# Kernel tuning notes

Hardware: AMD Instinct MI355X
Metric: run time of the kernel (lower is better)

Reference implementation:

```python
import jax, jax.numpy as jnp
import numpy as np

N_EMBED = 384

def setup_inputs() -> dict:
    key = jax.random.key(0)
    kx, kq, kk, kv = jax.random.split(key, 4)
    B, T, C = 512, 256, N_EMBED
    H = 64
    scale = 1.0 / np.sqrt(C)  # param init scale, keep activations sane
    x = jax.random.normal(kx, (B, T, C), dtype=jnp.float32)
    Wq = jax.random.normal(kq, (C, H), dtype=jnp.float32) * scale
    Wk = jax.random.normal(kk, (C, H), dtype=jnp.float32) * scale
    Wv = jax.random.normal(kv, (C, H), dtype=jnp.float32) * scale
    return {"x": x, "Wq": Wq, "Wk": Wk, "Wv": Wv}

def reference(x, Wq, Wk, Wv):
    B, T, C = x.shape
    q = jnp.einsum('btc,ch->bth', x, Wq)
    k = jnp.einsum('btc,ch->bth', x, Wk)
    v = jnp.einsum('btc,ch->bth', x, Wv)
    # NOTE: original scales by C**-0.5 with C = n_embed (384), not head_size.
    wei = jnp.einsum('bth,bsh->bts', q, k) * (C ** -0.5)  # [B,T,T]
    causal = jnp.tril(jnp.ones((T, T), dtype=bool))
    wei = jnp.where(causal, wei, -jnp.inf)
    wei = jax.nn.softmax(wei, axis=-1)
    out = jnp.einsum('bts,bsh->bth', wei, v)  # [B,T,H]
    return out
```

## Files before the change

### kernel.cpp

```cpp
#include <hip/hip_runtime.h>
#include <hip/hip_bf16.h>


constexpr int BSZ  = 512;
constexpr int TT   = 256;
constexpr int CDIM = 384;
constexpr int HDIM = 64;
constexpr int NQKV = 192;
constexpr float SCALE = 0.051031036307982884f;
constexpr int BTST = 392;

typedef __attribute__((ext_vector_type(8))) short bf16x8;
typedef __attribute__((ext_vector_type(4))) float f32x4;

__device__ inline unsigned short f2bf(float f) {
    __hip_bfloat16 h = __float2bfloat16(f);
    return *(unsigned short*)&h;
}
__device__ inline bf16x8 pack8(float4 a, float4 b) {
    unsigned short p[8] = { f2bf(a.x), f2bf(a.y), f2bf(a.z), f2bf(a.w),
                            f2bf(b.x), f2bf(b.y), f2bf(b.z), f2bf(b.w) };
    return *(bf16x8*)p;
}

__global__ __launch_bounds__(256) void prep_bt(
    const float* __restrict__ Wq, const float* __restrict__ Wk,
    const float* __restrict__ Wv, unsigned short* __restrict__ bt)
{
    int idx = blockIdx.x * 256 + threadIdx.x;
    if (idx >= NQKV * CDIM) return;
    int n = idx / CDIM, k = idx - n * CDIM;
    const float* W = (n < 64) ? Wq : (n < 128) ? Wk : Wv;
    bt[idx] = f2bf(W[(size_t)k * HDIM + (n & 63)]);
}

__global__ __launch_bounds__(1024) void fused(
    const float* __restrict__ x, const unsigned short* __restrict__ bt,
    float* __restrict__ out)
{
    __shared__ __align__(16) unsigned short smem[NQKV * BTST];
    unsigned short* btl = smem;
    unsigned short* qs  = smem;
    unsigned short* kl  = smem + 16384;
    unsigned short* vt  = smem + 32768;

    const int b = blockIdx.x, tid = threadIdx.x;
    const int w = tid >> 6, lane = tid & 63;
    const int lr = lane & 15, lk = lane >> 4;
    const float* xb = x + (size_t)b * TT * CDIM;

    for (int i = tid; i < NQKV * CDIM / 8; i += 1024) {
        int row = i / 48, c8 = i - row * 48;
        *(uint4*)&btl[row * BTST + c8 * 8] = ((const uint4*)bt)[i];
    }
    __syncthreads();

    const float* xrow = xb + (size_t)(16 * w + lr) * CDIM + lk * 8;

    f32x4 acc[12];
    #pragma unroll
    for (int ni = 0; ni < 12; ++ni) acc[ni] = (f32x4){0.f, 0.f, 0.f, 0.f};

    float4 f0 = *(const float4*)&xrow[0];
    float4 f1 = *(const float4*)&xrow[4];
    #pragma unroll 2
    for (int ks = 0; ks < 12; ++ks) {
        float4 c0 = f0, c1 = f1;
        if (ks < 11) {
            f0 = *(const float4*)&xrow[(ks + 1) * 32];
            f1 = *(const float4*)&xrow[(ks + 1) * 32 + 4];
        }
        bf16x8 a = pack8(c0, c1);
        #pragma unroll
        for (int ni = 0; ni < 12; ++ni) {
            bf16x8 bb = *(const bf16x8*)&btl[(ni * 16 + lr) * BTST + ks * 32 + lk * 8];
            acc[ni] = __builtin_amdgcn_mfma_f32_16x16x32_bf16(a, bb, acc[ni], 0, 0, 0);
        }
    }
    __syncthreads();

    unsigned short* pq = qs + w * 1024;
    #pragma unroll
    for (int ni = 0; ni < 4; ++ni)
        #pragma unroll
        for (int r = 0; r < 4; ++r) {
            int qr = lk * 4 + r;
            int h  = ni * 16 + lr;
            pq[qr * 64 + (h ^ ((qr & 7) << 3))] = f2bf(acc[ni][r] * SCALE);
        }
    #pragma unroll
    for (int ni = 4; ni < 8; ++ni)
        #pragma unroll
        for (int r = 0; r < 4; ++r) {
            int row = 16 * w + lk * 4 + r;
            int c2  = (ni - 4) * 16 + lr;
            kl[row * 64 + (c2 ^ ((row & 7) << 3))] = f2bf(acc[ni][r]);
        }
    #pragma unroll
    for (int ni = 8; ni < 12; ++ni) {
        int h  = (ni - 8) * 16 + lr;
        int t0 = 16 * w + lk * 4;
        unsigned short pk[4];
        #pragma unroll
        for (int r = 0; r < 4; ++r) pk[r] = f2bf(acc[ni][r]);
        *(uint2*)&vt[h * 256 + (t0 ^ ((h & 7) << 3))] = *(uint2*)pk;
    }
    __syncthreads();

    const int q0 = 16 * w;
    bf16x8 qa[2];
    #pragma unroll
    for (int kc = 0; kc < 2; ++kc)
        qa[kc] = *(const bf16x8*)&pq[lr * 64 + ((kc * 32 + lk * 8) ^ ((lr & 7) << 3))];

    f32x4 oacc[4];
    float mrow[4], lpart[4];
    #pragma unroll
    for (int nh = 0; nh < 4; ++nh) oacc[nh] = (f32x4){0.f, 0.f, 0.f, 0.f};
    #pragma unroll
    for (int r = 0; r < 4; ++r) { mrow[r] = -INFINITY; lpart[r] = 0.f; }

    const int lastt = w >> 2;
    for (int st = 0; st <= lastt; ++st) {
        f32x4 sa[4];
        #pragma unroll
        for (int ni = 0; ni < 4; ++ni) sa[ni] = (f32x4){0.f, 0.f, 0.f, 0.f};
        #pragma unroll
        for (int ni = 0; ni < 4; ++ni) {
            int row = st * 64 + ni * 16 + lr;
            #pragma unroll
            for (int kc = 0; kc < 2; ++kc) {
                bf16x8 kb = *(const bf16x8*)
                    &kl[row * 64 + ((kc * 32 + lk * 8) ^ ((lr & 7) << 3))];
                sa[ni] = __builtin_amdgcn_mfma_f32_16x16x32_bf16(qa[kc], kb, sa[ni], 0, 0, 0);
            }
        }
        if (st == lastt) {
            #pragma unroll
            for (int ni = 0; ni < 4; ++ni) {
                int sg = st * 64 + ni * 16 + lr;
                #pragma unroll
                for (int r = 0; r < 4; ++r) {
                    int qg = q0 + lk * 4 + r;
                    if (sg > qg) sa[ni][r] = -INFINITY;
                }
            }
        }
        float pm[4];
        #pragma unroll
        for (int r = 0; r < 4; ++r)
            pm[r] = fmaxf(fmaxf(sa[0][r], sa[1][r]), fmaxf(sa[2][r], sa[3][r]));
        #pragma unroll
        for (int stp = 1; stp < 16; stp <<= 1)
            #pragma unroll
            for (int r = 0; r < 4; ++r)
                pm[r] = fmaxf(pm[r], __shfl_xor(pm[r], stp));
        float mnew[4];
        #pragma unroll
        for (int r = 0; r < 4; ++r) {
            float mn = fmaxf(mrow[r], pm[r]);
            float corr = __expf(mrow[r] - mn);
            mrow[r] = mn; mnew[r] = mn;
            lpart[r] *= corr;
            #pragma unroll
            for (int nh = 0; nh < 4; ++nh) oacc[nh][r] *= corr;
        }
        #pragma unroll
        for (int ni = 0; ni < 4; ++ni) {
            int s = ni * 16 + lr;
            #pragma unroll
            for (int r = 0; r < 4; ++r) {
                float p = __expf(sa[ni][r] - mnew[r]);
                lpart[r] += p;
                int qr = lk * 4 + r;
                pq[qr * 64 + (s ^ ((qr & 7) << 3))] = f2bf(p);
            }
        }
        bf16x8 pa[2];
        #pragma unroll
        for (int kc = 0; kc < 2; ++kc)
            pa[kc] = *(const bf16x8*)
                &pq[lr * 64 + ((kc * 32 + lk * 8) ^ ((lr & 7) << 3))];
        #pragma unroll
        for (int nh = 0; nh < 4; ++nh) {
            int hrow = nh * 16 + lr;
            #pragma unroll
            for (int kc = 0; kc < 2; ++kc) {
                bf16x8 vb = *(const bf16x8*)
                    &vt[hrow * 256 + ((st * 64 + kc * 32 + lk * 8) ^ ((hrow & 7) << 3))];
                oacc[nh] = __builtin_amdgcn_mfma_f32_16x16x32_bf16(pa[kc], vb, oacc[nh], 0, 0, 0);
            }
        }
    }

    float linv[4];
    #pragma unroll
    for (int r = 0; r < 4; ++r) {
        float l = lpart[r];
        #pragma unroll
        for (int stp = 1; stp < 16; stp <<= 1) l += __shfl_xor(l, stp);
        linv[r] = 1.0f / l;
    }
    #pragma unroll
    for (int nh = 0; nh < 4; ++nh)
        #pragma unroll
        for (int r = 0; r < 4; ++r) {
            size_t row = (size_t)b * TT + q0 + lk * 4 + r;
            out[row * HDIM + nh * 16 + lr] = oacc[nh][r] * linv[r];
        }
}

extern "C" void kernel_launch(void* const* d_in, const int* in_sizes, int n_in,
                              void* d_out, int out_size, void* d_ws, size_t ws_size,
                              hipStream_t stream)
{
    const float* x  = (const float*)d_in[0];
    const float* Wq = (const float*)d_in[1];
    const float* Wk = (const float*)d_in[2];
    const float* Wv = (const float*)d_in[3];
    unsigned short* bt = (unsigned short*)d_ws;
    float* out = (float*)d_out;

    prep_bt<<<(NQKV * CDIM + 255) / 256, 256, 0, stream>>>(Wq, Wk, Wv, bt);
    fused<<<BSZ, 1024, 0, stream>>>(x, bt, out);
}
```

Baseline: 64.96 us.

## Halve block to 512 threads with two row tiles per wave and causal load balancing

The fused kernel now launches 512 threads per block, with launch bounds set for 2 blocks per CU. Each wave computes 32 rows of the QKV projection, reusing each weight fragment across two MFMA tiles, and prefetches x three steps ahead. In the attention phase each wave handles a pair of query tiles (w and 15-w) so causal work is balanced across waves. The cost is higher register pressure from doubled accumulators, which the 2-blocks-per-CU bound may force into spills. Occupancy also still depends on the large shared-memory allocation per block.

```diff
diff --git a/kernel.cpp b/kernel.cpp
--- a/kernel.cpp
+++ b/kernel.cpp
@@ -34,7 +34,7 @@
     bt[idx] = f2bf(W[(size_t)k * HDIM + (n & 63)]);
 }
 
-__global__ __launch_bounds__(1024) void fused(
+__global__ __launch_bounds__(512, 2) void fused(
     const float* __restrict__ x, const unsigned short* __restrict__ bt,
     float* __restrict__ out)
 {
@@ -49,165 +49,204 @@
     const int lr = lane & 15, lk = lane >> 4;
     const float* xb = x + (size_t)b * TT * CDIM;
 
-    for (int i = tid; i < NQKV * CDIM / 8; i += 1024) {
+    #pragma unroll
+    for (int p = 0; p < 18; ++p) {
+        int i = p * 512 + tid;
         int row = i / 48, c8 = i - row * 48;
         *(uint4*)&btl[row * BTST + c8 * 8] = ((const uint4*)bt)[i];
     }
     __syncthreads();
 
-    const float* xrow = xb + (size_t)(16 * w + lr) * CDIM + lk * 8;
-
-    f32x4 acc[12];
-    #pragma unroll
-    for (int ni = 0; ni < 12; ++ni) acc[ni] = (f32x4){0.f, 0.f, 0.f, 0.f};
-
-    float4 f0 = *(const float4*)&xrow[0];
-    float4 f1 = *(const float4*)&xrow[4];
-    #pragma unroll 2
-    for (int ks = 0; ks < 12; ++ks) {
-        float4 c0 = f0, c1 = f1;
-        if (ks < 11) {
-            f0 = *(const float4*)&xrow[(ks + 1) * 32];
-            f1 = *(const float4*)&xrow[(ks + 1) * 32 + 4];
+    const int m0 = 32 * w;
+    const float* xr0 = xb + (size_t)(m0 + lr) * CDIM + lk * 8;
+    const float* xr1 = xr0 + 16 * CDIM;
+
+    f32x4 acc0[12], acc1[12];
+    #pragma unroll
+    for (int ni = 0; ni < 12; ++ni) {
+        acc0[ni] = (f32x4){0.f, 0.f, 0.f, 0.f};
+        acc1[ni] = (f32x4){0.f, 0.f, 0.f, 0.f};
+    }
+
+    float4 pf0[4], pf1[4], pf2[4];
+#define LDCH(P, ks) { \
+    P[0] = *(const float4*)&xr0[(ks) * 32];     \
+    P[1] = *(const float4*)&xr0[(ks) * 32 + 4]; \
+    P[2] = *(const float4*)&xr1[(ks) * 32];     \
+    P[3] = *(const float4*)&xr1[(ks) * 32 + 4]; }
+#define STEP(P, ks, cond) { \
+    bf16x8 a0 = pack8(P[0], P[1]); \
+    bf16x8 a1 = pack8(P[2], P[3]); \
+    if (cond) LDCH(P, (ks) + 3); \
+    _Pragma("unroll") \
+    for (int ni = 0; ni < 12; ++ni) { \
+        bf16x8 bb = *(const bf16x8*)&btl[(ni * 16 + lr) * BTST + (ks) * 32 + lk * 8]; \
+        acc0[ni] = __builtin_amdgcn_mfma_f32_16x16x32_bf16(a0, bb, acc0[ni], 0, 0, 0); \
+        acc1[ni] = __builtin_amdgcn_mfma_f32_16x16x32_bf16(a1, bb, acc1[ni], 0, 0, 0); \
+    } }
+
+    LDCH(pf0, 0) LDCH(pf1, 1) LDCH(pf2, 2)
+    #pragma unroll
+    for (int kk = 0; kk < 4; ++kk) {
+        STEP(pf0, 3 * kk + 0, kk < 3)
+        STEP(pf1, 3 * kk + 1, kk < 3)
+        STEP(pf2, 3 * kk + 2, kk < 3)
+    }
+#undef LDCH
+#undef STEP
+    __syncthreads();
+
+    #pragma unroll
+    for (int mi = 0; mi < 2; ++mi) {
+        const f32x4* am = mi ? acc1 : acc0;
+        #pragma unroll
+        for (int ni = 0; ni < 4; ++ni)
+            #pragma unroll
+            for (int r = 0; r < 4; ++r) {
+                int row = m0 + mi * 16 + lk * 4 + r;
+                int h   = ni * 16 + lr;
+                qs[row * 64 + (h ^ ((row & 7) << 3))] = f2bf(am[ni][r] * SCALE);
+            }
+        #pragma unroll
+        for (int ni = 4; ni < 8; ++ni)
+            #pragma unroll
+            for (int r = 0; r < 4; ++r) {
+                int row = m0 + mi * 16 + lk * 4 + r;
+                int c2  = (ni - 4) * 16 + lr;
+                kl[row * 64 + (c2 ^ ((row & 7) << 3))] = f2bf(am[ni][r]);
+            }
+        #pragma unroll
+        for (int ni = 8; ni < 12; ++ni) {
+            int h  = (ni - 8) * 16 + lr;
+            int t0 = m0 + mi * 16 + lk * 4;
+            unsigned short pk[4];
+            #pragma unroll
+            for (int r = 0; r < 4; ++r) pk[r] = f2bf(am[ni][r]);
+            *(uint2*)&vt[h * 256 + (t0 ^ ((h & 7) << 3))] = *(uint2*)pk;
         }
-        bf16x8 a = pack8(c0, c1);
-        #pragma unroll
-        for (int ni = 0; ni < 12; ++ni) {
-            bf16x8 bb = *(const bf16x8*)&btl[(ni * 16 + lr) * BTST + ks * 32 + lk * 8];
-            acc[ni] = __builtin_amdgcn_mfma_f32_16x16x32_bf16(a, bb, acc[ni], 0, 0, 0);
+    }
+    __syncthreads();
+
+    const int q0a[2]  = {16 * w, 240 - 16 * w};
+    const int lastA[2] = {(q0a[0] + 15) >> 6, (q0a[1] + 15) >> 6};
+
+    bf16x8 qa[2][2];
+    #pragma unroll
+    for (int s2 = 0; s2 < 2; ++s2)
+        #pragma unroll
+        for (int kc = 0; kc < 2; ++kc)
+            qa[s2][kc] = *(const bf16x8*)
+                &qs[(q0a[s2] + lr) * 64 + ((kc * 32 + lk * 8) ^ ((lr & 7) << 3))];
+    unsigned short* pb = qs + w * 1024;
+
+    f32x4 oacc[2][4];
+    float mrow[2][4], lpart[2][4];
+    #pragma unroll
+    for (int s2 = 0; s2 < 2; ++s2) {
+        #pragma unroll
+        for (int nh = 0; nh < 4; ++nh) oacc[s2][nh] = (f32x4){0.f, 0.f, 0.f, 0.f};
+        #pragma unroll
+        for (int r = 0; r < 4; ++r) { mrow[s2][r] = -INFINITY; lpart[s2][r] = 0.f; }
+    }
+
+    for (int st = 0; st <= lastA[1]; ++st) {
+        #pragma unroll
+        for (int s2 = 0; s2 < 2; ++s2) {
+            if (st > lastA[s2]) continue;
+            const int q0 = q0a[s2];
+
+            f32x4 sa[4];
+            #pragma unroll
+            for (int ni = 0; ni < 4; ++ni) sa[ni] = (f32x4){0.f, 0.f, 0.f, 0.f};
+            #pragma unroll
+            for (int ni = 0; ni < 4; ++ni) {
+                int row = st * 64 + ni * 16 + lr;
+                #pragma unroll
+                for (int kc = 0; kc < 2; ++kc) {
+                    bf16x8 kb = *(const bf16x8*)
+                        &kl[row * 64 + ((kc * 32 + lk * 8) ^ ((lr & 7) << 3))];
+                    sa[ni] = __builtin_amdgcn_mfma_f32_16x16x32_bf16(
+                        qa[s2][kc], kb, sa[ni], 0, 0, 0);
+                }
+            }
+            if (st == lastA[s2]) {
+                #pragma unroll
+                for (int ni = 0; ni < 4; ++ni) {
+                    int sg = st * 64 + ni * 16 + lr;
+                    #pragma unroll
+                    for (int r = 0; r < 4; ++r) {
+                        int qg = q0 + lk * 4 + r;
+                        if (sg > qg) sa[ni][r] = -INFINITY;
+                    }
+                }
+            }
+            float pm[4];
+            #pragma unroll
+            for (int r = 0; r < 4; ++r)
+                pm[r] = fmaxf(fmaxf(sa[0][r], sa[1][r]), fmaxf(sa[2][r], sa[3][r]));
+            #pragma unroll
+            for (int stp = 1; stp < 16; stp <<= 1)
+                #pragma unroll
+                for (int r = 0; r < 4; ++r)
+                    pm[r] = fmaxf(pm[r], __shfl_xor(pm[r], stp));
+            float mnew[4];
+            #pragma unroll
+            for (int r = 0; r < 4; ++r) {
+                float mn = fmaxf(mrow[s2][r], pm[r]);
+                float corr = __expf(mrow[s2][r] - mn);
+                mrow[s2][r] = mn; mnew[r] = mn;
+                lpart[s2][r] *= corr;
+                #pragma unroll
+                for (int nh = 0; nh < 4; ++nh) oacc[s2][nh][r] *= corr;
+            }
+            #pragma unroll
+            for (int ni = 0; ni < 4; ++ni) {
+                int s = ni * 16 + lr;
+                #pragma unroll
+                for (int r = 0; r < 4; ++r) {
+                    float p = __expf(sa[ni][r] - mnew[r]);
+                    lpart[s2][r] += p;
+                    int qr = lk * 4 + r;
+                    pb[qr * 64 + (s ^ ((qr & 7) << 3))] = f2bf(p);
+                }
+            }
+            bf16x8 pa[2];
+            #pragma unroll
+            for (int kc = 0; kc < 2; ++kc)
+                pa[kc] = *(const bf16x8*)
+                    &pb[lr * 64 + ((kc * 32 + lk * 8) ^ ((lr & 7) << 3))];
+            #pragma unroll
+            for (int nh = 0; nh < 4; ++nh) {
+                int hrow = nh * 16 + lr;
+                #pragma unroll
+                for (int kc = 0; kc < 2; ++kc) {
+                    bf16x8 vb = *(const bf16x8*)
+                        &vt[hrow * 256 + ((st * 64 + kc * 32 + lk * 8) ^ ((hrow & 7) << 3))];
+                    oacc[s2][nh] = __builtin_amdgcn_mfma_f32_16x16x32_bf16(
+                        pa[kc], vb, oacc[s2][nh], 0, 0, 0);
+                }
+            }
         }
     }
-    __syncthreads();
-
-    unsigned short* pq = qs + w * 1024;
-    #pragma unroll
-    for (int ni = 0; ni < 4; ++ni)
+
+    #pragma unroll
+    for (int s2 = 0; s2 < 2; ++s2) {
+        float linv[4];
         #pragma unroll
         for (int r = 0; r < 4; ++r) {
-            int qr = lk * 4 + r;
-            int h  = ni * 16 + lr;
-            pq[qr * 64 + (h ^ ((qr & 7) << 3))] = f2bf(acc[ni][r] * SCALE);
+            float l = lpart[s2][r];
+            #pragma unroll
+            for (int stp = 1; stp < 16; stp <<= 1) l += __shfl_xor(l, stp);
+            linv[r] = 1.0f / l;
         }
-    #pragma unroll
-    for (int ni = 4; ni < 8; ++ni)
-        #pragma unroll
-        for (int r = 0; r < 4; ++r) {
-            int row = 16 * w + lk * 4 + r;
-            int c2  = (ni - 4) * 16 + lr;
-            kl[row * 64 + (c2 ^ ((row & 7) << 3))] = f2bf(acc[ni][r]);
-        }
-    #pragma unroll
-    for (int ni = 8; ni < 12; ++ni) {
-        int h  = (ni - 8) * 16 + lr;
-        int t0 = 16 * w + lk * 4;
-        unsigned short pk[4];
-        #pragma unroll
-        for (int r = 0; r < 4; ++r) pk[r] = f2bf(acc[ni][r]);
-        *(uint2*)&vt[h * 256 + (t0 ^ ((h & 7) << 3))] = *(uint2*)pk;
-    }
-    __syncthreads();
-
-    const int q0 = 16 * w;
-    bf16x8 qa[2];
-    #pragma unroll
-    for (int kc = 0; kc < 2; ++kc)
-        qa[kc] = *(const bf16x8*)&pq[lr * 64 + ((kc * 32 + lk * 8) ^ ((lr & 7) << 3))];
-
-    f32x4 oacc[4];
-    float mrow[4], lpart[4];
-    #pragma unroll
-    for (int nh = 0; nh < 4; ++nh) oacc[nh] = (f32x4){0.f, 0.f, 0.f, 0.f};
-    #pragma unroll
-    for (int r = 0; r < 4; ++r) { mrow[r] = -INFINITY; lpart[r] = 0.f; }
-
-    const int lastt = w >> 2;
-    for (int st = 0; st <= lastt; ++st) {
-        f32x4 sa[4];
-        #pragma unroll
-        for (int ni = 0; ni < 4; ++ni) sa[ni] = (f32x4){0.f, 0.f, 0.f, 0.f};
-        #pragma unroll
-        for (int ni = 0; ni < 4; ++ni) {
-            int row = st * 64 + ni * 16 + lr;
-            #pragma unroll
-            for (int kc = 0; kc < 2; ++kc) {
-                bf16x8 kb = *(const bf16x8*)
-                    &kl[row * 64 + ((kc * 32 + lk * 8) ^ ((lr & 7) << 3))];
-                sa[ni] = __builtin_amdgcn_mfma_f32_16x16x32_bf16(qa[kc], kb, sa[ni], 0, 0, 0);
-            }
-        }
-        if (st == lastt) {
-            #pragma unroll
-            for (int ni = 0; ni < 4; ++ni) {
-                int sg = st * 64 + ni * 16 + lr;
-                #pragma unroll
-                for (int r = 0; r < 4; ++r) {
-                    int qg = q0 + lk * 4 + r;
-                    if (sg > qg) sa[ni][r] = -INFINITY;
-                }
-            }
-        }
-        float pm[4];
-        #pragma unroll
-        for (int r = 0; r < 4; ++r)
-            pm[r] = fmaxf(fmaxf(sa[0][r], sa[1][r]), fmaxf(sa[2][r], sa[3][r]));
-        #pragma unroll
-        for (int stp = 1; stp < 16; stp <<= 1)
-            #pragma unroll
-            for (int r = 0; r < 4; ++r)
-                pm[r] = fmaxf(pm[r], __shfl_xor(pm[r], stp));
-        float mnew[4];
-        #pragma unroll
-        for (int r = 0; r < 4; ++r) {
-            float mn = fmaxf(mrow[r], pm[r]);
-            float corr = __expf(mrow[r] - mn);
-            mrow[r] = mn; mnew[r] = mn;
-            lpart[r] *= corr;
-            #pragma unroll
-            for (int nh = 0; nh < 4; ++nh) oacc[nh][r] *= corr;
-        }
-        #pragma unroll
-        for (int ni = 0; ni < 4; ++ni) {
-            int s = ni * 16 + lr;
-            #pragma unroll
-            for (int r = 0; r < 4; ++r) {
-                float p = __expf(sa[ni][r] - mnew[r]);
-                lpart[r] += p;
-                int qr = lk * 4 + r;
-                pq[qr * 64 + (s ^ ((qr & 7) << 3))] = f2bf(p);
-            }
-        }
-        bf16x8 pa[2];
-        #pragma unroll
-        for (int kc = 0; kc < 2; ++kc)
-            pa[kc] = *(const bf16x8*)
-                &pq[lr * 64 + ((kc * 32 + lk * 8) ^ ((lr & 7) << 3))];
-        #pragma unroll
-        for (int nh = 0; nh < 4; ++nh) {
-            int hrow = nh * 16 + lr;
-            #pragma unroll
-            for (int kc = 0; kc < 2; ++kc) {
-                bf16x8 vb = *(const bf16x8*)
-                    &vt[hrow * 256 + ((st * 64 + kc * 32 + lk * 8) ^ ((hrow & 7) << 3))];
-                oacc[nh] = __builtin_amdgcn_mfma_f32_16x16x32_bf16(pa[kc], vb, oacc[nh], 0, 0, 0);
-            }
-        }
-    }
-
-    float linv[4];
-    #pragma unroll
-    for (int r = 0; r < 4; ++r) {
-        float l = lpart[r];
-        #pragma unroll
-        for (int stp = 1; stp < 16; stp <<= 1) l += __shfl_xor(l, stp);
-        linv[r] = 1.0f / l;
-    }
-    #pragma unroll
-    for (int nh = 0; nh < 4; ++nh)
-        #pragma unroll
-        for (int r = 0; r < 4; ++r) {
-            size_t row = (size_t)b * TT + q0 + lk * 4 + r;
-            out[row * HDIM + nh * 16 + lr] = oacc[nh][r] * linv[r];
-        }
+        #pragma unroll
+        for (int nh = 0; nh < 4; ++nh)
+            #pragma unroll
+            for (int r = 0; r < 4; ++r) {
+                size_t row = (size_t)b * TT + q0a[s2] + lk * 4 + r;
+                out[row * HDIM + nh * 16 + lr] = oacc[s2][nh][r] * linv[r];
+            }
+    }
 }
 
 extern "C" void kernel_launch(void* const* d_in, const int* in_sizes, int n_in,
@@ -222,5 +261,5 @@
     float* out = (float*)d_out;
 
     prep_bt<<<(NQKV * CDIM + 255) / 256, 256, 0, stream>>>(Wq, Wk, Wv, bt);
-    fused<<<BSZ, 1024, 0, stream>>>(x, bt, out);
-}
+    fused<<<BSZ, 512, 0, stream>>>(x, bt, out);
+}
```

After: 66.77 us. +2.8%, slower.
